# Kernel optimization log

Hardware: AMD Instinct MI355X
Metric: run time of the kernel (lower is better)

The kernel has to match this reference:

```python
import jax, jax.numpy as jnp
import numpy as np

NUM_NODES = 100000
NUM_EDGES = 1600000
NUM_GRAPHS = 64
IN_DIM, HID, NCLS = 64, 128, 10


def setup_inputs() -> dict:
    key = jax.random.key(0)
    ks = jax.random.split(key, 12)
    x = jax.random.normal(ks[0], (NUM_NODES, IN_DIM), dtype=jnp.float32)
    src = jax.random.randint(ks[1], (NUM_EDGES,), 0, NUM_NODES, dtype=jnp.int32)
    dst = jax.random.randint(ks[2], (NUM_EDGES,), 0, NUM_NODES, dtype=jnp.int32)
    batch = jnp.sort(jax.random.randint(ks[3], (NUM_NODES,), 0, NUM_GRAPHS, dtype=jnp.int32))
    def glorot(k, shape):
        lim = (6.0 / (shape[0] + shape[1])) ** 0.5
        return jax.random.uniform(k, shape, jnp.float32, -lim, lim)
    return {
        "x": x, "src": src, "dst": dst, "batch": batch,
        "W1": glorot(ks[4], (IN_DIM, HID)), "b1": jnp.zeros((HID,), jnp.float32),
        "W2": glorot(ks[5], (HID, HID)), "b2": jnp.zeros((HID,), jnp.float32),
        "Wl1": glorot(ks[6], (HID, HID // 2)), "bl1": jnp.zeros((HID // 2,), jnp.float32),
        "Wl2": glorot(ks[7], (HID // 2, NCLS)), "bl2": jnp.zeros((NCLS,), jnp.float32),
    }


def gcn_conv(x, W, b, src, dst):
    # GCNConv: out = D^{-1/2} (A + I) D^{-1/2} (x @ W) + b, deg from A+I
    h = x @ W  # [N, H]
    ones = jnp.ones((src.shape[0],), h.dtype)
    deg = jax.ops.segment_sum(ones, dst, num_segments=NUM_NODES) + 1.0  # +1 self-loop
    dinv = jax.lax.rsqrt(deg)  # [N]
    norm = dinv[src] * dinv[dst]  # [E]
    msg = h[src] * norm[:, None]  # [E, H] gather + scale
    agg = jax.ops.segment_sum(msg, dst, num_segments=NUM_NODES)  # scatter-add
    agg = agg + h * (dinv * dinv)[:, None]  # self-loop message
    return agg + b


def reference(x, src, dst, batch, W1, b1, W2, b2, Wl1, bl1, Wl2, bl2):
    h = jax.nn.relu(gcn_conv(x, W1, b1, src, dst))
    h = jax.nn.relu(gcn_conv(h, W2, b2, src, dst))
    # global mean pool per graph
    sums = jax.ops.segment_sum(h, batch, num_segments=NUM_GRAPHS)  # [G, H]
    cnts = jax.ops.segment_sum(jnp.ones((h.shape[0],), h.dtype), batch, num_segments=NUM_GRAPHS)
    pooled = sums / jnp.maximum(cnts, 1.0)[:, None]
    h = jax.nn.relu(pooled @ Wl1 + bl1)
    return h @ Wl2 + bl2  # [G, num_classes]
```

## Files before the change

### kernel.cpp

```cpp
#include <hip/hip_runtime.h>
#include <hip/hip_bf16.h>

#define NODES_N 100000
#define EDGES_E 1600000
#define GRAPHS_G 64

#define BIN_SHIFT 7
#define BIN_NODES 128
#define NBINS 782
#define NB1 512
#define EPB1 3125

typedef unsigned int uint;
typedef unsigned short ushort;
typedef __attribute__((ext_vector_type(8))) short bf16x8;
typedef __attribute__((ext_vector_type(4))) float f32x4;


__device__ inline uint pack_bf2(float lo, float hi) {
    __hip_bfloat162 h2 = __float22bfloat162_rn(make_float2(lo, hi));
    return *reinterpret_cast<uint*>(&h2);
}

__device__ inline void acc_bf2(uint w, float& a0, float& a1) {
    a0 += __uint_as_float(w << 16);
    a1 += __uint_as_float(w & 0xffff0000u);
}

__device__ inline ushort f2bf(float v) {
    __hip_bfloat16 b = __float2bfloat16(v);
    return *reinterpret_cast<ushort*>(&b);
}


__global__ __launch_bounds__(256) void p1_hist_k(const int* __restrict__ dst,
                                                 int* __restrict__ hist_t) {
    __shared__ int h[NBINS];
    for (int i = threadIdx.x; i < NBINS; i += 256) h[i] = 0;
    __syncthreads();
    int b = blockIdx.x;
    int e0 = b * EPB1, e1 = min(EDGES_E, e0 + EPB1);
    for (int e = e0 + threadIdx.x; e < e1; e += 256)
        atomicAdd(&h[dst[e] >> BIN_SHIFT], 1);
    __syncthreads();
    for (int i = threadIdx.x; i < NBINS; i += 256)
        hist_t[i * NB1 + b] = h[i];
}

__global__ __launch_bounds__(256) void p1_scanbins_k(int* __restrict__ hist_t,
                                                     int* __restrict__ bintot) {
    __shared__ int sd[256];
    __shared__ int carry;
    int bin = blockIdx.x, t = threadIdx.x;
    if (t == 0) carry = 0;
    __syncthreads();
    int* row = hist_t + bin * NB1;
    for (int base = 0; base < NB1; base += 256) {
        int v = row[base + t];
        sd[t] = v; __syncthreads();
        for (int o = 1; o < 256; o <<= 1) {
            int x = (t >= o) ? sd[t - o] : 0;
            __syncthreads();
            sd[t] += x;
            __syncthreads();
        }
        row[base + t] = carry + sd[t] - v;
        __syncthreads();
        if (t == 255) carry += sd[255];
        __syncthreads();
    }
    if (t == 0) bintot[bin] = carry;
}

__global__ __launch_bounds__(1024) void binstart_k(const int* __restrict__ bintot,
                                                   int* __restrict__ binstart,
                                                   int* __restrict__ rowptr) {
    __shared__ int sd[1024];
    int t = threadIdx.x;
    int v = (t < NBINS) ? bintot[t] : 0;
    sd[t] = v; __syncthreads();
    for (int o = 1; o < 1024; o <<= 1) {
        int x = (t >= o) ? sd[t - o] : 0;
        __syncthreads();
        sd[t] += x;
        __syncthreads();
    }
    if (t < NBINS) binstart[t] = sd[t] - v;
    if (t == 0) { binstart[NBINS] = EDGES_E; rowptr[NODES_N] = EDGES_E; }
}

__global__ __launch_bounds__(256) void p1_scatter_k(const int* __restrict__ src,
                                                    const int* __restrict__ dst,
                                                    const int* __restrict__ hist_t,
                                                    const int* __restrict__ binstart,
                                                    uint* __restrict__ pairs) {
    __shared__ int cur[NBINS];
    int b = blockIdx.x;
    for (int i = threadIdx.x; i < NBINS; i += 256)
        cur[i] = binstart[i] + hist_t[i * NB1 + b];
    __syncthreads();
    int e0 = b * EPB1, e1 = min(EDGES_E, e0 + EPB1);
    for (int e = e0 + threadIdx.x; e < e1; e += 256) {
        int d = dst[e];
        int pos = atomicAdd(&cur[d >> BIN_SHIFT], 1);
        pairs[pos] = ((uint)src[e] << BIN_SHIFT) | (uint)(d & (BIN_NODES - 1));
    }
}

__global__ __launch_bounds__(256) void p2_build_k(const uint* __restrict__ pairs,
                                                  const int* __restrict__ binstart,
                                                  int* __restrict__ colidx,
                                                  int* __restrict__ rowptr,
                                                  float* __restrict__ dinv) {
    __shared__ int h[BIN_NODES];
    __shared__ int off[BIN_NODES];
    __shared__ int cur[BIN_NODES];
    int bin = blockIdx.x, t = threadIdx.x;
    int node0 = bin << BIN_SHIFT;
    if (t < BIN_NODES) h[t] = 0;
    __syncthreads();
    int e0 = binstart[bin], e1 = binstart[bin + 1];
    for (int e = e0 + t; e < e1; e += 256)
        atomicAdd(&h[pairs[e] & (BIN_NODES - 1)], 1);
    __syncthreads();
    if (t < BIN_NODES) off[t] = h[t];
    __syncthreads();
    for (int o = 1; o < BIN_NODES; o <<= 1) {
        int x = (t < BIN_NODES && t >= o) ? off[t - o] : 0;
        __syncthreads();
        if (t < BIN_NODES) off[t] += x;
        __syncthreads();
    }
    if (t < BIN_NODES) {
        int excl = off[t] - h[t];
        cur[t] = e0 + excl;
        int node = node0 + t;
        if (node < NODES_N) {
            rowptr[node] = e0 + excl;
            dinv[node] = rsqrtf((float)h[t] + 1.0f);
        }
    }
    __syncthreads();
    for (int e = e0 + t; e < e1; e += 256) {
        uint p = pairs[e];
        int pos = atomicAdd(&cur[p & (BIN_NODES - 1)], 1);
        colidx[pos] = (int)(p >> BIN_SHIFT);
    }
}


__global__ __launch_bounds__(256) void scale_x_k(const float* __restrict__ x,
                                                 const float* __restrict__ dinv,
                                                 uint* __restrict__ xt, int n) {
    int gid = blockIdx.x * blockDim.x + threadIdx.x;
    if (gid >= n * 8) return;
    int row = gid >> 3, l = gid & 7;
    float dv = dinv[row];
    const float* p = &x[(size_t)row * 64 + l * 8];
    float4 a = *(const float4*)p;
    float4 b = *(const float4*)(p + 4);
    uint4 o;
    o.x = pack_bf2(a.x * dv, a.y * dv);
    o.y = pack_bf2(a.z * dv, a.w * dv);
    o.z = pack_bf2(b.x * dv, b.y * dv);
    o.w = pack_bf2(b.z * dv, b.w * dv);
    *(uint4*)&xt[(size_t)row * 32 + l * 4] = o;
}


__global__ __launch_bounds__(256) void gather64_k(const uint* __restrict__ xt,
                                                  const int* __restrict__ rowptr,
                                                  const int* __restrict__ colidx,
                                                  uint* __restrict__ st, int n) {
    int lane = threadIdx.x & 7;
    int local = threadIdx.x >> 3;
    int co = lane * 4;
    for (int node = blockIdx.x * 32 + local; node < n; node += gridDim.x * 32) {
        float a0=0,a1=0,a2=0,a3=0,a4=0,a5=0,a6=0,a7=0;
        uint4 v = *(const uint4*)&xt[(size_t)node * 32 + co];
        acc_bf2(v.x, a0, a1); acc_bf2(v.y, a2, a3);
        acc_bf2(v.z, a4, a5); acc_bf2(v.w, a6, a7);
        int beg = rowptr[node], end = rowptr[node + 1];
        int e = beg;
        for (; e + 3 < end; e += 4) {
            int s0 = colidx[e], s1 = colidx[e+1], s2 = colidx[e+2], s3 = colidx[e+3];
            uint4 v0 = *(const uint4*)&xt[(size_t)s0 * 32 + co];
            uint4 v1 = *(const uint4*)&xt[(size_t)s1 * 32 + co];
            uint4 v2 = *(const uint4*)&xt[(size_t)s2 * 32 + co];
            uint4 v3 = *(const uint4*)&xt[(size_t)s3 * 32 + co];
            acc_bf2(v0.x,a0,a1); acc_bf2(v0.y,a2,a3); acc_bf2(v0.z,a4,a5); acc_bf2(v0.w,a6,a7);
            acc_bf2(v1.x,a0,a1); acc_bf2(v1.y,a2,a3); acc_bf2(v1.z,a4,a5); acc_bf2(v1.w,a6,a7);
            acc_bf2(v2.x,a0,a1); acc_bf2(v2.y,a2,a3); acc_bf2(v2.z,a4,a5); acc_bf2(v2.w,a6,a7);
            acc_bf2(v3.x,a0,a1); acc_bf2(v3.y,a2,a3); acc_bf2(v3.z,a4,a5); acc_bf2(v3.w,a6,a7);
        }
        for (; e < end; e++) {
            uint4 v0 = *(const uint4*)&xt[(size_t)colidx[e] * 32 + co];
            acc_bf2(v0.x,a0,a1); acc_bf2(v0.y,a2,a3); acc_bf2(v0.z,a4,a5); acc_bf2(v0.w,a6,a7);
        }
        uint4 o;
        o.x = pack_bf2(a0, a1);
        o.y = pack_bf2(a2, a3);
        o.z = pack_bf2(a4, a5);
        o.w = pack_bf2(a6, a7);
        *(uint4*)&st[(size_t)node * 32 + co] = o;
    }
}


template <int P>
__global__ __launch_bounds__(256) void gather128_k(const uint* __restrict__ hp,
                                                   const int* __restrict__ rowptr,
                                                   const int* __restrict__ colidx,
                                                   const float* __restrict__ dinv,
                                                   const float* __restrict__ bias,
                                                   uint* __restrict__ h2b, int n) {
    int lane = threadIdx.x & 7;
    int local = threadIdx.x >> 3;
    int co = P * 32 + lane * 4;
    for (int node = blockIdx.x * 32 + local; node < n; node += gridDim.x * 32) {
        float a0=0,a1=0,a2=0,a3=0,a4=0,a5=0,a6=0,a7=0;
        uint4 v = *(const uint4*)&hp[(size_t)node * 64 + co];
        acc_bf2(v.x, a0, a1); acc_bf2(v.y, a2, a3);
        acc_bf2(v.z, a4, a5); acc_bf2(v.w, a6, a7);
        int beg = rowptr[node], end = rowptr[node + 1];
        int e = beg;
        for (; e + 3 < end; e += 4) {
            int s0 = colidx[e], s1 = colidx[e+1], s2 = colidx[e+2], s3 = colidx[e+3];
            uint4 v0 = *(const uint4*)&hp[(size_t)s0 * 64 + co];
            uint4 v1 = *(const uint4*)&hp[(size_t)s1 * 64 + co];
            uint4 v2 = *(const uint4*)&hp[(size_t)s2 * 64 + co];
            uint4 v3 = *(const uint4*)&hp[(size_t)s3 * 64 + co];
            acc_bf2(v0.x,a0,a1); acc_bf2(v0.y,a2,a3); acc_bf2(v0.z,a4,a5); acc_bf2(v0.w,a6,a7);
            acc_bf2(v1.x,a0,a1); acc_bf2(v1.y,a2,a3); acc_bf2(v1.z,a4,a5); acc_bf2(v1.w,a6,a7);
            acc_bf2(v2.x,a0,a1); acc_bf2(v2.y,a2,a3); acc_bf2(v2.z,a4,a5); acc_bf2(v2.w,a6,a7);
            acc_bf2(v3.x,a0,a1); acc_bf2(v3.y,a2,a3); acc_bf2(v3.z,a4,a5); acc_bf2(v3.w,a6,a7);
        }
        for (; e < end; e++) {
            uint4 v0 = *(const uint4*)&hp[(size_t)colidx[e] * 64 + co];
            acc_bf2(v0.x,a0,a1); acc_bf2(v0.y,a2,a3); acc_bf2(v0.z,a4,a5); acc_bf2(v0.w,a6,a7);
        }
        float dv = dinv[node];
        int jb = P * 64 + lane * 8;
        float4 b0 = *(const float4*)&bias[jb];
        float4 b1 = *(const float4*)&bias[jb + 4];
        float o0 = fmaxf(fmaf(dv, a0, b0.x), 0.f);
        float o1 = fmaxf(fmaf(dv, a1, b0.y), 0.f);
        float o2 = fmaxf(fmaf(dv, a2, b0.z), 0.f);
        float o3 = fmaxf(fmaf(dv, a3, b0.w), 0.f);
        float o4 = fmaxf(fmaf(dv, a4, b1.x), 0.f);
        float o5 = fmaxf(fmaf(dv, a5, b1.y), 0.f);
        float o6 = fmaxf(fmaf(dv, a6, b1.z), 0.f);
        float o7 = fmaxf(fmaf(dv, a7, b1.w), 0.f);
        uint4 ov;
        ov.x = pack_bf2(o0, o1);
        ov.y = pack_bf2(o2, o3);
        ov.z = pack_bf2(o4, o5);
        ov.w = pack_bf2(o6, o7);
        *(uint4*)&h2b[(size_t)node * 64 + co] = ov;
    }
}


__device__ inline void pack_w_one(const float* W, ushort* Wf, int gid, int KS) {
    int j = gid & 7, l = (gid >> 3) & 63, f = gid >> 9;
    int nt = f / KS, ks = f - nt * KS;
    int k = ks * 32 + ((l >> 4) & 3) * 8 + j;
    int n = nt * 16 + (l & 15);
    Wf[gid] = f2bf(W[k * 128 + n]);
}

__global__ void pack_w_both_k(const float* __restrict__ W1, ushort* __restrict__ W1f,
                              const float* __restrict__ W2, ushort* __restrict__ W2f) {
    int gid = blockIdx.x * 256 + threadIdx.x;
    if (gid < 8192) pack_w_one(W1, W1f, gid, 2);
    else if (gid < 8192 + 16384) pack_w_one(W2, W2f, gid - 8192, 4);
}


template <int K, int EPI>
__global__ __launch_bounds__(256) void gemm_mfma_k(const ushort* __restrict__ A,
                                                   const ushort* __restrict__ Wf,
                                                   const float* __restrict__ dinv,
                                                   const float* __restrict__ bias,
                                                   ushort* __restrict__ outb, int n) {
    constexpr int KS = K / 32;
    int wave = threadIdx.x >> 6;
    int lane = threadIdx.x & 63;
    int row0 = (blockIdx.x * 4 + wave) * 16;
    if (row0 >= n) return;
    int m = lane & 15, g = lane >> 4;
    int arow = min(row0 + m, n - 1);

    bf16x8 a[KS];
    const ushort* abase = &A[(size_t)arow * K + g * 8];
#pragma unroll
    for (int ks = 0; ks < KS; ks++)
        a[ks] = *reinterpret_cast<const bf16x8*>(abase + ks * 32);

    f32x4 acc[8];
#pragma unroll
    for (int nt = 0; nt < 8; nt++) {
        acc[nt] = (f32x4){0.f, 0.f, 0.f, 0.f};
#pragma unroll
        for (int ks = 0; ks < KS; ks++) {
            bf16x8 b = *reinterpret_cast<const bf16x8*>(&Wf[((size_t)(nt * KS + ks) * 64 + lane) * 8]);
            acc[nt] = __builtin_amdgcn_mfma_f32_16x16x32_bf16(a[ks], b, acc[nt], 0, 0, 0);
        }
    }

    int orow0 = row0 + g * 4;
#pragma unroll
    for (int r = 0; r < 4; r++) {
        int row = orow0 + r;
        if (row < n) {
            float dvr = dinv[row];
#pragma unroll
            for (int nt = 0; nt < 8; nt++) {
                float v = acc[nt][r] * dvr;
                if (EPI == 0) v = fmaxf(v + bias[nt * 16 + m], 0.f);
                outb[(size_t)row * 128 + nt * 16 + m] = f2bf(v);
            }
        }
    }
}


__global__ __launch_bounds__(128) void pool_k(const uint* __restrict__ h2b,
                                              const int* __restrict__ batch, int n,
                                              float* __restrict__ sums, float* __restrict__ cnts) {
    int j = threadIdx.x;
    int wj = j >> 1;
    int hi = j & 1;
    int chunk = (n + gridDim.x - 1) / gridDim.x;
    int i0 = blockIdx.x * chunk;
    int i1 = min(n, i0 + chunk);
    if (i0 >= n) return;
    int cur = batch[i0];
    float acc = 0.f;
    int cnt = 0;
    for (int i = i0; i < i1; i++) {
        int g = batch[i];
        if (g != cur) {
            atomicAdd(&sums[cur * 128 + j], acc);
            if (j == 0) atomicAdd(&cnts[cur], (float)cnt);
            acc = 0.f; cnt = 0; cur = g;
        }
        uint w = h2b[(size_t)i * 64 + wj];
        acc += __uint_as_float(hi ? (w & 0xffff0000u) : (w << 16));
        cnt++;
    }
    atomicAdd(&sums[cur * 128 + j], acc);
    if (j == 0) atomicAdd(&cnts[cur], (float)cnt);
}


__global__ __launch_bounds__(64) void mlp_k(const float* __restrict__ sums, const float* __restrict__ cnts,
                                            const float* __restrict__ Wl1, const float* __restrict__ bl1,
                                            const float* __restrict__ Wl2, const float* __restrict__ bl2,
                                            float* __restrict__ out) {
    __shared__ float pooled[128];
    __shared__ float hidden[64];
    int g = blockIdx.x, t = threadIdx.x;
    float c = fmaxf(cnts[g], 1.0f);
    pooled[t]      = sums[g * 128 + t] / c;
    pooled[t + 64] = sums[g * 128 + 64 + t] / c;
    __syncthreads();
    float a = bl1[t];
#pragma unroll 4
    for (int cc = 0; cc < 128; cc++) a = fmaf(pooled[cc], Wl1[cc * 64 + t], a);
    hidden[t] = fmaxf(a, 0.f);
    __syncthreads();
    if (t < 10) {
        float o = bl2[t];
#pragma unroll 8
        for (int jj = 0; jj < 64; jj++) o = fmaf(hidden[jj], Wl2[jj * 10 + t], o);
        out[g * 10 + t] = o;
    }
}


extern "C" void kernel_launch(void* const* d_in, const int* in_sizes, int n_in,
                              void* d_out, int out_size, void* d_ws, size_t ws_size,
                              hipStream_t stream) {
    const float* x    = (const float*)d_in[0];
    const int*   src  = (const int*)d_in[1];
    const int*   dst  = (const int*)d_in[2];
    const int*   batch= (const int*)d_in[3];
    const float* W1   = (const float*)d_in[4];
    const float* b1   = (const float*)d_in[5];
    const float* W2   = (const float*)d_in[6];
    const float* b2   = (const float*)d_in[7];
    const float* Wl1  = (const float*)d_in[8];
    const float* bl1  = (const float*)d_in[9];
    const float* Wl2  = (const float*)d_in[10];
    const float* bl2  = (const float*)d_in[11];
    float* out = (float*)d_out;

    const int N = NODES_N;

    size_t off = 0;
    auto take = [&](size_t bytes) { size_t o = off; off = (off + bytes + 255) & ~(size_t)255; return o; };
    char* ws = (char*)d_ws;
    ushort* h1b  = (ushort*)(ws + take((size_t)N * 128 * 2));
    uint*   h2p  = (uint*)(ws + take((size_t)N * 128 * 2));
    size_t  shbytes = (size_t)N * 64 * 2;
    char*   shreg = ws + take(shbytes);
    uint*   pairs = (uint*)shreg;
    uint*   stil  = (uint*)shreg;
    uint*   xt   = (uint*)(ws + take((size_t)N * 64 * 2));
    float*  dinv = (float*)(ws + take((size_t)N * 4));
    ushort* W1f  = (ushort*)(ws + take((size_t)64 * 128 * 2));
    ushort* W2f  = (ushort*)(ws + take((size_t)128 * 128 * 2));
    size_t zbytes = ((size_t)GRAPHS_G * 128 + GRAPHS_G) * 4;
    char*  zbase  = ws + take(zbytes);
    float* sums   = (float*)zbase;
    float* cnts   = (float*)(zbase + (size_t)GRAPHS_G * 128 * 4);
    int*   rowptr = (int*)(ws + take((size_t)(N + 1) * 4));
    int*   colidx = (int*)(ws + take((size_t)EDGES_E * 4));
    int*   hist_t = (int*)(ws + take((size_t)NBINS * NB1 * 4));
    int*   bintot = (int*)(ws + take((size_t)NBINS * 4));
    int*   binstart = (int*)(ws + take((size_t)(NBINS + 1) * 4));
    uint*  h2b = (uint*)h1b;
    (void)ws_size; (void)in_sizes; (void)n_in; (void)out_size;

    hipMemsetAsync(zbase, 0, zbytes, stream);

    pack_w_both_k<<<(8192 + 16384 + 255) / 256, 256, 0, stream>>>(W1, W1f, W2, W2f);

    p1_hist_k<<<NB1, 256, 0, stream>>>(dst, hist_t);
    p1_scanbins_k<<<NBINS, 256, 0, stream>>>(hist_t, bintot);
    binstart_k<<<1, 1024, 0, stream>>>(bintot, binstart, rowptr);
    p1_scatter_k<<<NB1, 256, 0, stream>>>(src, dst, hist_t, binstart, pairs);
    p2_build_k<<<NBINS, 256, 0, stream>>>(pairs, binstart, colidx, rowptr, dinv);

    scale_x_k<<<(N * 8 + 255) / 256, 256, 0, stream>>>(x, dinv, xt, N);
    gather64_k<<<2048, 256, 0, stream>>>(xt, rowptr, colidx, stil, N);
    int gblk = (N + 63) / 64;
    gemm_mfma_k<64, 0><<<gblk, 256, 0, stream>>>((const ushort*)stil, W1f, dinv, b1, h1b, N);

    gemm_mfma_k<128, 1><<<gblk, 256, 0, stream>>>(h1b, W2f, dinv, nullptr, (ushort*)h2p, N);
    int g128 = (N + 31) / 32;
    gather128_k<0><<<g128, 256, 0, stream>>>(h2p, rowptr, colidx, dinv, b2, h2b, N);
    gather128_k<1><<<g128, 256, 0, stream>>>(h2p, rowptr, colidx, dinv, b2, h2b, N);

    pool_k<<<1024, 128, 0, stream>>>(h2b, batch, N, sums, cnts);
    mlp_k<<<GRAPHS_G, 64, 0, stream>>>(sums, cnts, Wl1, bl1, Wl2, bl2, out);
}
```

Before: 236.9 us.

## Fuse x scaling into CSR build and gather64 into layer-1 MFMA GEMM

The dinv scaling and bf16 packing of x now happen at the end of p2_build_k, which drops the separate scale_x kernel. The layer-1 neighbor gather is folded into the MFMA GEMM: each lane aggregates the 16 features it feeds into the MFMA A operand, so the intermediate gathered buffer never goes through global memory. The weight packing and the zeroing of the pool accumulators are merged into one kernel that replaces the memset. The cost is that the fused gather assigns one node per 4 lanes with 2×16B loads each, which changes the memory access granularity and occupancy compared with the 8-lanes-per-node gather.

```diff
diff --git a/kernel.cpp b/kernel.cpp
--- a/kernel.cpp
+++ b/kernel.cpp
@@ -30,6 +30,27 @@
 __device__ inline ushort f2bf(float v) {
     __hip_bfloat16 b = __float2bfloat16(v);
     return *reinterpret_cast<ushort*>(&b);
+}
+
+
+__device__ inline void pack_w_one(const float* W, ushort* Wf, int gid, int KS) {
+    int j = gid & 7, l = (gid >> 3) & 63, f = gid >> 9;
+    int nt = f / KS, ks = f - nt * KS;
+    int k = ks * 32 + ((l >> 4) & 3) * 8 + j;
+    int n = nt * 16 + (l & 15);
+    Wf[gid] = f2bf(W[k * 128 + n]);
+}
+
+__global__ void pack_w_zero_k(const float* __restrict__ W1, ushort* __restrict__ W1f,
+                              const float* __restrict__ W2, ushort* __restrict__ W2f,
+                              float* __restrict__ zf) {
+    int gid = blockIdx.x * 256 + threadIdx.x;
+    if (gid < 8192) pack_w_one(W1, W1f, gid, 2);
+    else if (gid < 24576) pack_w_one(W2, W2f, gid - 8192, 4);
+    else {
+        int i = gid - 24576;
+        if (i < GRAPHS_G * 128 + GRAPHS_G) zf[i] = 0.f;
+    }
 }
 
 
@@ -109,12 +130,15 @@
 
 __global__ __launch_bounds__(256) void p2_build_k(const uint* __restrict__ pairs,
                                                   const int* __restrict__ binstart,
+                                                  const float* __restrict__ x,
                                                   int* __restrict__ colidx,
                                                   int* __restrict__ rowptr,
-                                                  float* __restrict__ dinv) {
+                                                  float* __restrict__ dinv,
+                                                  uint* __restrict__ xt) {
     __shared__ int h[BIN_NODES];
     __shared__ int off[BIN_NODES];
     __shared__ int cur[BIN_NODES];
+    __shared__ float ldv[BIN_NODES];
     int bin = blockIdx.x, t = threadIdx.x;
     int node0 = bin << BIN_SHIFT;
     if (t < BIN_NODES) h[t] = 0;
@@ -126,18 +150,20 @@
     if (t < BIN_NODES) off[t] = h[t];
     __syncthreads();
     for (int o = 1; o < BIN_NODES; o <<= 1) {
-        int x = (t < BIN_NODES && t >= o) ? off[t - o] : 0;
-        __syncthreads();
-        if (t < BIN_NODES) off[t] += x;
+        int x2 = (t < BIN_NODES && t >= o) ? off[t - o] : 0;
+        __syncthreads();
+        if (t < BIN_NODES) off[t] += x2;
         __syncthreads();
     }
     if (t < BIN_NODES) {
         int excl = off[t] - h[t];
         cur[t] = e0 + excl;
+        float dv = rsqrtf((float)h[t] + 1.0f);
+        ldv[t] = dv;
         int node = node0 + t;
         if (node < NODES_N) {
             rowptr[node] = e0 + excl;
-            dinv[node] = rsqrtf((float)h[t] + 1.0f);
+            dinv[node] = dv;
         }
     }
     __syncthreads();
@@ -146,63 +172,128 @@
         int pos = atomicAdd(&cur[p & (BIN_NODES - 1)], 1);
         colidx[pos] = (int)(p >> BIN_SHIFT);
     }
-}
-
-
-__global__ __launch_bounds__(256) void scale_x_k(const float* __restrict__ x,
-                                                 const float* __restrict__ dinv,
-                                                 uint* __restrict__ xt, int n) {
-    int gid = blockIdx.x * blockDim.x + threadIdx.x;
-    if (gid >= n * 8) return;
-    int row = gid >> 3, l = gid & 7;
-    float dv = dinv[row];
-    const float* p = &x[(size_t)row * 64 + l * 8];
-    float4 a = *(const float4*)p;
-    float4 b = *(const float4*)(p + 4);
-    uint4 o;
-    o.x = pack_bf2(a.x * dv, a.y * dv);
-    o.y = pack_bf2(a.z * dv, a.w * dv);
-    o.z = pack_bf2(b.x * dv, b.y * dv);
-    o.w = pack_bf2(b.z * dv, b.w * dv);
-    *(uint4*)&xt[(size_t)row * 32 + l * 4] = o;
-}
-
-
-__global__ __launch_bounds__(256) void gather64_k(const uint* __restrict__ xt,
-                                                  const int* __restrict__ rowptr,
-                                                  const int* __restrict__ colidx,
-                                                  uint* __restrict__ st, int n) {
-    int lane = threadIdx.x & 7;
-    int local = threadIdx.x >> 3;
-    int co = lane * 4;
-    for (int node = blockIdx.x * 32 + local; node < n; node += gridDim.x * 32) {
-        float a0=0,a1=0,a2=0,a3=0,a4=0,a5=0,a6=0,a7=0;
-        uint4 v = *(const uint4*)&xt[(size_t)node * 32 + co];
-        acc_bf2(v.x, a0, a1); acc_bf2(v.y, a2, a3);
-        acc_bf2(v.z, a4, a5); acc_bf2(v.w, a6, a7);
-        int beg = rowptr[node], end = rowptr[node + 1];
-        int e = beg;
-        for (; e + 3 < end; e += 4) {
-            int s0 = colidx[e], s1 = colidx[e+1], s2 = colidx[e+2], s3 = colidx[e+3];
-            uint4 v0 = *(const uint4*)&xt[(size_t)s0 * 32 + co];
-            uint4 v1 = *(const uint4*)&xt[(size_t)s1 * 32 + co];
-            uint4 v2 = *(const uint4*)&xt[(size_t)s2 * 32 + co];
-            uint4 v3 = *(const uint4*)&xt[(size_t)s3 * 32 + co];
-            acc_bf2(v0.x,a0,a1); acc_bf2(v0.y,a2,a3); acc_bf2(v0.z,a4,a5); acc_bf2(v0.w,a6,a7);
-            acc_bf2(v1.x,a0,a1); acc_bf2(v1.y,a2,a3); acc_bf2(v1.z,a4,a5); acc_bf2(v1.w,a6,a7);
-            acc_bf2(v2.x,a0,a1); acc_bf2(v2.y,a2,a3); acc_bf2(v2.z,a4,a5); acc_bf2(v2.w,a6,a7);
-            acc_bf2(v3.x,a0,a1); acc_bf2(v3.y,a2,a3); acc_bf2(v3.z,a4,a5); acc_bf2(v3.w,a6,a7);
-        }
-        for (; e < end; e++) {
-            uint4 v0 = *(const uint4*)&xt[(size_t)colidx[e] * 32 + co];
-            acc_bf2(v0.x,a0,a1); acc_bf2(v0.y,a2,a3); acc_bf2(v0.z,a4,a5); acc_bf2(v0.w,a6,a7);
-        }
-        uint4 o;
-        o.x = pack_bf2(a0, a1);
-        o.y = pack_bf2(a2, a3);
-        o.z = pack_bf2(a4, a5);
-        o.w = pack_bf2(a6, a7);
-        *(uint4*)&st[(size_t)node * 32 + co] = o;
+    int nmax = min(NODES_N - node0, BIN_NODES);
+    for (int i = t; i < nmax * 16; i += 256) {
+        int nl = i >> 4, c = i & 15;
+        int node = node0 + nl;
+        float dv = ldv[nl];
+        float4 v = *(const float4*)&x[(size_t)node * 64 + c * 4];
+        uint2 o = make_uint2(pack_bf2(v.x * dv, v.y * dv), pack_bf2(v.z * dv, v.w * dv));
+        *(uint2*)&xt[(size_t)node * 32 + c * 2] = o;
+    }
+}
+
+
+__global__ __launch_bounds__(256) void conv1_fused_k(const uint* __restrict__ xt,
+                                                     const int* __restrict__ rowptr,
+                                                     const int* __restrict__ colidx,
+                                                     const float* __restrict__ dinv,
+                                                     const float* __restrict__ bias,
+                                                     const ushort* __restrict__ Wf,
+                                                     ushort* __restrict__ h1b, int n) {
+    int wave = threadIdx.x >> 6;
+    int lane = threadIdx.x & 63;
+    int row0 = (blockIdx.x * 4 + wave) * 16;
+    if (row0 >= n) return;
+    int m = lane & 15, g = lane >> 4;
+    int node = min(row0 + m, n - 1);
+    int g4 = g * 4;
+
+    float s[16];
+#pragma unroll
+    for (int i = 0; i < 16; i++) s[i] = 0.f;
+
+    auto accrow = [&](int r) {
+        uint4 vA = *(const uint4*)&xt[(size_t)r * 32 + g4];
+        uint4 vB = *(const uint4*)&xt[(size_t)r * 32 + 16 + g4];
+        acc_bf2(vA.x, s[0], s[1]);  acc_bf2(vA.y, s[2], s[3]);
+        acc_bf2(vA.z, s[4], s[5]);  acc_bf2(vA.w, s[6], s[7]);
+        acc_bf2(vB.x, s[8], s[9]);  acc_bf2(vB.y, s[10], s[11]);
+        acc_bf2(vB.z, s[12], s[13]); acc_bf2(vB.w, s[14], s[15]);
+    };
+
+    accrow(node);
+    int beg = rowptr[node], end = rowptr[node + 1];
+    int e = beg;
+    for (; e + 3 < end; e += 4) {
+        int s0 = colidx[e], s1 = colidx[e + 1], s2 = colidx[e + 2], s3 = colidx[e + 3];
+        accrow(s0); accrow(s1); accrow(s2); accrow(s3);
+    }
+    for (; e < end; e++) accrow(colidx[e]);
+
+    uint4 u0 = make_uint4(pack_bf2(s[0], s[1]), pack_bf2(s[2], s[3]),
+                          pack_bf2(s[4], s[5]), pack_bf2(s[6], s[7]));
+    uint4 u1 = make_uint4(pack_bf2(s[8], s[9]), pack_bf2(s[10], s[11]),
+                          pack_bf2(s[12], s[13]), pack_bf2(s[14], s[15]));
+    bf16x8 a0 = *reinterpret_cast<bf16x8*>(&u0);
+    bf16x8 a1 = *reinterpret_cast<bf16x8*>(&u1);
+
+    f32x4 acc[8];
+#pragma unroll
+    for (int nt = 0; nt < 8; nt++) {
+        acc[nt] = (f32x4){0.f, 0.f, 0.f, 0.f};
+        bf16x8 b0 = *reinterpret_cast<const bf16x8*>(&Wf[((size_t)(nt * 2 + 0) * 64 + lane) * 8]);
+        bf16x8 b1 = *reinterpret_cast<const bf16x8*>(&Wf[((size_t)(nt * 2 + 1) * 64 + lane) * 8]);
+        acc[nt] = __builtin_amdgcn_mfma_f32_16x16x32_bf16(a0, b0, acc[nt], 0, 0, 0);
+        acc[nt] = __builtin_amdgcn_mfma_f32_16x16x32_bf16(a1, b1, acc[nt], 0, 0, 0);
+    }
+
+    int orow0 = row0 + g * 4;
+#pragma unroll
+    for (int r = 0; r < 4; r++) {
+        int row = orow0 + r;
+        if (row < n) {
+            float dvr = dinv[row];
+#pragma unroll
+            for (int nt = 0; nt < 8; nt++) {
+                float v = fmaxf(fmaf(dvr, acc[nt][r], bias[nt * 16 + m]), 0.f);
+                h1b[(size_t)row * 128 + nt * 16 + m] = f2bf(v);
+            }
+        }
+    }
+}
+
+
+template <int K>
+__global__ __launch_bounds__(256) void gemm_mfma_k(const ushort* __restrict__ A,
+                                                   const ushort* __restrict__ Wf,
+                                                   const float* __restrict__ dinv,
+                                                   ushort* __restrict__ outb, int n) {
+    constexpr int KS = K / 32;
+    int wave = threadIdx.x >> 6;
+    int lane = threadIdx.x & 63;
+    int row0 = (blockIdx.x * 4 + wave) * 16;
+    if (row0 >= n) return;
+    int m = lane & 15, g = lane >> 4;
+    int arow = min(row0 + m, n - 1);
+
+    bf16x8 a[KS];
+    const ushort* abase = &A[(size_t)arow * K + g * 8];
+#pragma unroll
+    for (int ks = 0; ks < KS; ks++)
+        a[ks] = *reinterpret_cast<const bf16x8*>(abase + ks * 32);
+
+    f32x4 acc[8];
+#pragma unroll
+    for (int nt = 0; nt < 8; nt++) {
+        acc[nt] = (f32x4){0.f, 0.f, 0.f, 0.f};
+#pragma unroll
+        for (int ks = 0; ks < KS; ks++) {
+            bf16x8 b = *reinterpret_cast<const bf16x8*>(&Wf[((size_t)(nt * KS + ks) * 64 + lane) * 8]);
+            acc[nt] = __builtin_amdgcn_mfma_f32_16x16x32_bf16(a[ks], b, acc[nt], 0, 0, 0);
+        }
+    }
+
+    int orow0 = row0 + g * 4;
+#pragma unroll
+    for (int r = 0; r < 4; r++) {
+        int row = orow0 + r;
+        if (row < n) {
+            float dvr = dinv[row];
+#pragma unroll
+            for (int nt = 0; nt < 8; nt++)
+                outb[(size_t)row * 128 + nt * 16 + m] = f2bf(acc[nt][r] * dvr);
+        }
     }
 }
 
@@ -261,70 +352,6 @@
 }
 
 
-__device__ inline void pack_w_one(const float* W, ushort* Wf, int gid, int KS) {
-    int j = gid & 7, l = (gid >> 3) & 63, f = gid >> 9;
-    int nt = f / KS, ks = f - nt * KS;
-    int k = ks * 32 + ((l >> 4) & 3) * 8 + j;
-    int n = nt * 16 + (l & 15);
-    Wf[gid] = f2bf(W[k * 128 + n]);
-}
-
-__global__ void pack_w_both_k(const float* __restrict__ W1, ushort* __restrict__ W1f,
-                              const float* __restrict__ W2, ushort* __restrict__ W2f) {
-    int gid = blockIdx.x * 256 + threadIdx.x;
-    if (gid < 8192) pack_w_one(W1, W1f, gid, 2);
-    else if (gid < 8192 + 16384) pack_w_one(W2, W2f, gid - 8192, 4);
-}
-
-
-template <int K, int EPI>
-__global__ __launch_bounds__(256) void gemm_mfma_k(const ushort* __restrict__ A,
-                                                   const ushort* __restrict__ Wf,
-                                                   const float* __restrict__ dinv,
-                                                   const float* __restrict__ bias,
-                                                   ushort* __restrict__ outb, int n) {
-    constexpr int KS = K / 32;
-    int wave = threadIdx.x >> 6;
-    int lane = threadIdx.x & 63;
-    int row0 = (blockIdx.x * 4 + wave) * 16;
-    if (row0 >= n) return;
-    int m = lane & 15, g = lane >> 4;
-    int arow = min(row0 + m, n - 1);
-
-    bf16x8 a[KS];
-    const ushort* abase = &A[(size_t)arow * K + g * 8];
-#pragma unroll
-    for (int ks = 0; ks < KS; ks++)
-        a[ks] = *reinterpret_cast<const bf16x8*>(abase + ks * 32);
-
-    f32x4 acc[8];
-#pragma unroll
-    for (int nt = 0; nt < 8; nt++) {
-        acc[nt] = (f32x4){0.f, 0.f, 0.f, 0.f};
-#pragma unroll
-        for (int ks = 0; ks < KS; ks++) {
-            bf16x8 b = *reinterpret_cast<const bf16x8*>(&Wf[((size_t)(nt * KS + ks) * 64 + lane) * 8]);
-            acc[nt] = __builtin_amdgcn_mfma_f32_16x16x32_bf16(a[ks], b, acc[nt], 0, 0, 0);
-        }
-    }
-
-    int orow0 = row0 + g * 4;
-#pragma unroll
-    for (int r = 0; r < 4; r++) {
-        int row = orow0 + r;
-        if (row < n) {
-            float dvr = dinv[row];
-#pragma unroll
-            for (int nt = 0; nt < 8; nt++) {
-                float v = acc[nt][r] * dvr;
-                if (EPI == 0) v = fmaxf(v + bias[nt * 16 + m], 0.f);
-                outb[(size_t)row * 128 + nt * 16 + m] = f2bf(v);
-            }
-        }
-    }
-}
-
-
 __global__ __launch_bounds__(128) void pool_k(const uint* __restrict__ h2b,
                                               const int* __restrict__ batch, int n,
                                               float* __restrict__ sums, float* __restrict__ cnts) {
@@ -403,10 +430,7 @@
     char* ws = (char*)d_ws;
     ushort* h1b  = (ushort*)(ws + take((size_t)N * 128 * 2));
     uint*   h2p  = (uint*)(ws + take((size_t)N * 128 * 2));
-    size_t  shbytes = (size_t)N * 64 * 2;
-    char*   shreg = ws + take(shbytes);
-    uint*   pairs = (uint*)shreg;
-    uint*   stil  = (uint*)shreg;
+    uint*   pairs = (uint*)(ws + take((size_t)EDGES_E * 4));
     uint*   xt   = (uint*)(ws + take((size_t)N * 64 * 2));
     float*  dinv = (float*)(ws + take((size_t)N * 4));
     ushort* W1f  = (ushort*)(ws + take((size_t)64 * 128 * 2));
@@ -423,22 +447,19 @@
     uint*  h2b = (uint*)h1b;
     (void)ws_size; (void)in_sizes; (void)n_in; (void)out_size;
 
-    hipMemsetAsync(zbase, 0, zbytes, stream);
-
-    pack_w_both_k<<<(8192 + 16384 + 255) / 256, 256, 0, stream>>>(W1, W1f, W2, W2f);
+    pack_w_zero_k<<<(24576 + GRAPHS_G * 128 + GRAPHS_G + 255) / 256, 256, 0, stream>>>(
+        W1, W1f, W2, W2f, sums);
 
     p1_hist_k<<<NB1, 256, 0, stream>>>(dst, hist_t);
     p1_scanbins_k<<<NBINS, 256, 0, stream>>>(hist_t, bintot);
     binstart_k<<<1, 1024, 0, stream>>>(bintot, binstart, rowptr);
     p1_scatter_k<<<NB1, 256, 0, stream>>>(src, dst, hist_t, binstart, pairs);
-    p2_build_k<<<NBINS, 256, 0, stream>>>(pairs, binstart, colidx, rowptr, dinv);
-
-    scale_x_k<<<(N * 8 + 255) / 256, 256, 0, stream>>>(x, dinv, xt, N);
-    gather64_k<<<2048, 256, 0, stream>>>(xt, rowptr, colidx, stil, N);
+    p2_build_k<<<NBINS, 256, 0, stream>>>(pairs, binstart, x, colidx, rowptr, dinv, xt);
+
     int gblk = (N + 63) / 64;
-    gemm_mfma_k<64, 0><<<gblk, 256, 0, stream>>>((const ushort*)stil, W1f, dinv, b1, h1b, N);
-
-    gemm_mfma_k<128, 1><<<gblk, 256, 0, stream>>>(h1b, W2f, dinv, nullptr, (ushort*)h2p, N);
+    conv1_fused_k<<<gblk, 256, 0, stream>>>(xt, rowptr, colidx, dinv, b1, W1f, h1b, N);
+
+    gemm_mfma_k<128><<<gblk, 256, 0, stream>>>(h1b, W2f, dinv, (ushort*)h2p, N);
     int g128 = (N + 31) / 32;
     gather128_k<0><<<g128, 256, 0, stream>>>(h2p, rowptr, colidx, dinv, b2, h2b, N);
     gather128_k<1><<<g128, 256, 0, stream>>>(h2p, rowptr, colidx, dinv, b2, h2b, N);
```

Result: no change. 235.7 us (-0.5%).

## Fuse layer GEMMs, fold x scaling into CSR build, merge launches

Applied to the files above, without the earlier changes.

The two MFMA GEMMs become one kernel that keeps the layer-1 output in LDS and feeds it straight into the layer-2 GEMM, so the h1 round trip through global memory goes away. The dinv scaling and bf16 packing of x now happen inside p2_build_k, and the memset is folded into the weight-packing kernel. The two gather128 launches become a single 2D grid, and the gather kernels move from grid-stride loops to one node per thread group. Together these cut kernel launches and intermediate traffic, at the cost of more registers and LDS in the fused GEMM.

```diff
diff --git a/kernel.cpp b/kernel.cpp
--- a/kernel.cpp
+++ b/kernel.cpp
@@ -30,6 +30,29 @@
 __device__ inline ushort f2bf(float v) {
     __hip_bfloat16 b = __float2bfloat16(v);
     return *reinterpret_cast<ushort*>(&b);
+}
+
+
+__device__ inline void pack_w_one(const float* W, ushort* Wf, int gid, int KS) {
+    int j = gid & 7, l = (gid >> 3) & 63, f = gid >> 9;
+    int nt = f / KS, ks = f - nt * KS;
+    int k = ks * 32 + ((l >> 4) & 3) * 8 + j;
+    int n = nt * 16 + (l & 15);
+    Wf[gid] = f2bf(W[k * 128 + n]);
+}
+
+#define NZERO (GRAPHS_G * 128 + GRAPHS_G)
+
+__global__ void pack_w_zero_k(const float* __restrict__ W1, ushort* __restrict__ W1f,
+                              const float* __restrict__ W2, ushort* __restrict__ W2f,
+                              float* __restrict__ zf) {
+    int gid = blockIdx.x * 256 + threadIdx.x;
+    if (gid < 8192) pack_w_one(W1, W1f, gid, 2);
+    else if (gid < 24576) pack_w_one(W2, W2f, gid - 8192, 4);
+    else {
+        int i = gid - 24576;
+        if (i < NZERO) zf[i] = 0.f;
+    }
 }
 
 
@@ -109,12 +132,15 @@
 
 __global__ __launch_bounds__(256) void p2_build_k(const uint* __restrict__ pairs,
                                                   const int* __restrict__ binstart,
+                                                  const float* __restrict__ x,
                                                   int* __restrict__ colidx,
                                                   int* __restrict__ rowptr,
-                                                  float* __restrict__ dinv) {
+                                                  float* __restrict__ dinv,
+                                                  uint* __restrict__ xt) {
     __shared__ int h[BIN_NODES];
     __shared__ int off[BIN_NODES];
     __shared__ int cur[BIN_NODES];
+    __shared__ float ldv[BIN_NODES];
     int bin = blockIdx.x, t = threadIdx.x;
     int node0 = bin << BIN_SHIFT;
     if (t < BIN_NODES) h[t] = 0;
@@ -126,18 +152,20 @@
     if (t < BIN_NODES) off[t] = h[t];
     __syncthreads();
     for (int o = 1; o < BIN_NODES; o <<= 1) {
-        int x = (t < BIN_NODES && t >= o) ? off[t - o] : 0;
-        __syncthreads();
-        if (t < BIN_NODES) off[t] += x;
+        int x2 = (t < BIN_NODES && t >= o) ? off[t - o] : 0;
+        __syncthreads();
+        if (t < BIN_NODES) off[t] += x2;
         __syncthreads();
     }
     if (t < BIN_NODES) {
         int excl = off[t] - h[t];
         cur[t] = e0 + excl;
+        float dv = rsqrtf((float)h[t] + 1.0f);
+        ldv[t] = dv;
         int node = node0 + t;
         if (node < NODES_N) {
             rowptr[node] = e0 + excl;
-            dinv[node] = rsqrtf((float)h[t] + 1.0f);
+            dinv[node] = dv;
         }
     }
     __syncthreads();
@@ -146,25 +174,15 @@
         int pos = atomicAdd(&cur[p & (BIN_NODES - 1)], 1);
         colidx[pos] = (int)(p >> BIN_SHIFT);
     }
-}
-
-
-__global__ __launch_bounds__(256) void scale_x_k(const float* __restrict__ x,
-                                                 const float* __restrict__ dinv,
-                                                 uint* __restrict__ xt, int n) {
-    int gid = blockIdx.x * blockDim.x + threadIdx.x;
-    if (gid >= n * 8) return;
-    int row = gid >> 3, l = gid & 7;
-    float dv = dinv[row];
-    const float* p = &x[(size_t)row * 64 + l * 8];
-    float4 a = *(const float4*)p;
-    float4 b = *(const float4*)(p + 4);
-    uint4 o;
-    o.x = pack_bf2(a.x * dv, a.y * dv);
-    o.y = pack_bf2(a.z * dv, a.w * dv);
-    o.z = pack_bf2(b.x * dv, b.y * dv);
-    o.w = pack_bf2(b.z * dv, b.w * dv);
-    *(uint4*)&xt[(size_t)row * 32 + l * 4] = o;
+    int nmax = min(NODES_N - node0, BIN_NODES);
+    for (int i = t; i < nmax * 16; i += 256) {
+        int nl = i >> 4, c = i & 15;
+        int node = node0 + nl;
+        float dv = ldv[nl];
+        float4 v = *(const float4*)&x[(size_t)node * 64 + c * 4];
+        uint2 o = make_uint2(pack_bf2(v.x * dv, v.y * dv), pack_bf2(v.z * dv, v.w * dv));
+        *(uint2*)&xt[(size_t)node * 32 + c * 2] = o;
+    }
 }
 
 
@@ -175,7 +193,9 @@
     int lane = threadIdx.x & 7;
     int local = threadIdx.x >> 3;
     int co = lane * 4;
-    for (int node = blockIdx.x * 32 + local; node < n; node += gridDim.x * 32) {
+    int node = blockIdx.x * 32 + local;
+    if (node >= n) return;
+    {
         float a0=0,a1=0,a2=0,a3=0,a4=0,a5=0,a6=0,a7=0;
         uint4 v = *(const uint4*)&xt[(size_t)node * 32 + co];
         acc_bf2(v.x, a0, a1); acc_bf2(v.y, a2, a3);
@@ -207,17 +227,90 @@
 }
 
 
-template <int P>
+__global__ __launch_bounds__(256) void gemm_dual_k(const ushort* __restrict__ A,
+                                                   const ushort* __restrict__ W1f,
+                                                   const ushort* __restrict__ W2f,
+                                                   const float* __restrict__ dinv,
+                                                   const float* __restrict__ b1,
+                                                   ushort* __restrict__ h2p, int n) {
+    __shared__ ushort hl[4][16][132];
+    int wave = threadIdx.x >> 6;
+    int lane = threadIdx.x & 63;
+    int row0 = (blockIdx.x * 4 + wave) * 16;
+    if (row0 >= n) return;
+    int m = lane & 15, g = lane >> 4;
+    int arow = min(row0 + m, n - 1);
+
+    const ushort* ab = &A[(size_t)arow * 64 + g * 8];
+    bf16x8 a0 = *reinterpret_cast<const bf16x8*>(ab);
+    bf16x8 a1 = *reinterpret_cast<const bf16x8*>(ab + 32);
+    f32x4 acc[8];
+#pragma unroll
+    for (int nt = 0; nt < 8; nt++) {
+        acc[nt] = (f32x4){0.f, 0.f, 0.f, 0.f};
+        bf16x8 w0 = *reinterpret_cast<const bf16x8*>(&W1f[((size_t)(nt * 2 + 0) * 64 + lane) * 8]);
+        bf16x8 w1 = *reinterpret_cast<const bf16x8*>(&W1f[((size_t)(nt * 2 + 1) * 64 + lane) * 8]);
+        acc[nt] = __builtin_amdgcn_mfma_f32_16x16x32_bf16(a0, w0, acc[nt], 0, 0, 0);
+        acc[nt] = __builtin_amdgcn_mfma_f32_16x16x32_bf16(a1, w1, acc[nt], 0, 0, 0);
+    }
+
+    int orow0 = row0 + g * 4;
+#pragma unroll
+    for (int r = 0; r < 4; r++) {
+        float dvr = dinv[min(orow0 + r, n - 1)];
+#pragma unroll
+        for (int nt = 0; nt < 8; nt++) {
+            float v = fmaxf(fmaf(dvr, acc[nt][r], b1[nt * 16 + m]), 0.f);
+            hl[wave][g * 4 + r][nt * 16 + m] = f2bf(v);
+        }
+    }
+
+    bf16x8 hfrag[4];
+#pragma unroll
+    for (int ks = 0; ks < 4; ks++) {
+        uint2 lo = *(const uint2*)&hl[wave][m][g * 8 + ks * 32];
+        uint2 hi = *(const uint2*)&hl[wave][m][g * 8 + ks * 32 + 4];
+        uint4 u = make_uint4(lo.x, lo.y, hi.x, hi.y);
+        hfrag[ks] = *reinterpret_cast<bf16x8*>(&u);
+    }
+
+    f32x4 acc2[8];
+#pragma unroll
+    for (int nt = 0; nt < 8; nt++) {
+        acc2[nt] = (f32x4){0.f, 0.f, 0.f, 0.f};
+#pragma unroll
+        for (int ks = 0; ks < 4; ks++) {
+            bf16x8 w = *reinterpret_cast<const bf16x8*>(&W2f[((size_t)(nt * 4 + ks) * 64 + lane) * 8]);
+            acc2[nt] = __builtin_amdgcn_mfma_f32_16x16x32_bf16(hfrag[ks], w, acc2[nt], 0, 0, 0);
+        }
+    }
+
+#pragma unroll
+    for (int r = 0; r < 4; r++) {
+        int row = orow0 + r;
+        if (row < n) {
+            float dvr = dinv[row];
+#pragma unroll
+            for (int nt = 0; nt < 8; nt++)
+                h2p[(size_t)row * 128 + nt * 16 + m] = f2bf(acc2[nt][r] * dvr);
+        }
+    }
+}
+
+
 __global__ __launch_bounds__(256) void gather128_k(const uint* __restrict__ hp,
                                                    const int* __restrict__ rowptr,
                                                    const int* __restrict__ colidx,
                                                    const float* __restrict__ dinv,
                                                    const float* __restrict__ bias,
                                                    uint* __restrict__ h2b, int n) {
+    int P = blockIdx.y;
     int lane = threadIdx.x & 7;
     int local = threadIdx.x >> 3;
     int co = P * 32 + lane * 4;
-    for (int node = blockIdx.x * 32 + local; node < n; node += gridDim.x * 32) {
+    int node = blockIdx.x * 32 + local;
+    if (node >= n) return;
+    {
         float a0=0,a1=0,a2=0,a3=0,a4=0,a5=0,a6=0,a7=0;
         uint4 v = *(const uint4*)&hp[(size_t)node * 64 + co];
         acc_bf2(v.x, a0, a1); acc_bf2(v.y, a2, a3);
@@ -257,70 +350,6 @@
         ov.z = pack_bf2(o4, o5);
         ov.w = pack_bf2(o6, o7);
         *(uint4*)&h2b[(size_t)node * 64 + co] = ov;
-    }
-}
-
-
-__device__ inline void pack_w_one(const float* W, ushort* Wf, int gid, int KS) {
-    int j = gid & 7, l = (gid >> 3) & 63, f = gid >> 9;
-    int nt = f / KS, ks = f - nt * KS;
-    int k = ks * 32 + ((l >> 4) & 3) * 8 + j;
-    int n = nt * 16 + (l & 15);
-    Wf[gid] = f2bf(W[k * 128 + n]);
-}
-
-__global__ void pack_w_both_k(const float* __restrict__ W1, ushort* __restrict__ W1f,
-                              const float* __restrict__ W2, ushort* __restrict__ W2f) {
-    int gid = blockIdx.x * 256 + threadIdx.x;
-    if (gid < 8192) pack_w_one(W1, W1f, gid, 2);
-    else if (gid < 8192 + 16384) pack_w_one(W2, W2f, gid - 8192, 4);
-}
-
-
-template <int K, int EPI>
-__global__ __launch_bounds__(256) void gemm_mfma_k(const ushort* __restrict__ A,
-                                                   const ushort* __restrict__ Wf,
-                                                   const float* __restrict__ dinv,
-                                                   const float* __restrict__ bias,
-                                                   ushort* __restrict__ outb, int n) {
-    constexpr int KS = K / 32;
-    int wave = threadIdx.x >> 6;
-    int lane = threadIdx.x & 63;
-    int row0 = (blockIdx.x * 4 + wave) * 16;
-    if (row0 >= n) return;
-    int m = lane & 15, g = lane >> 4;
-    int arow = min(row0 + m, n - 1);
-
-    bf16x8 a[KS];
-    const ushort* abase = &A[(size_t)arow * K + g * 8];
-#pragma unroll
-    for (int ks = 0; ks < KS; ks++)
-        a[ks] = *reinterpret_cast<const bf16x8*>(abase + ks * 32);
-
-    f32x4 acc[8];
-#pragma unroll
-    for (int nt = 0; nt < 8; nt++) {
-        acc[nt] = (f32x4){0.f, 0.f, 0.f, 0.f};
-#pragma unroll
-        for (int ks = 0; ks < KS; ks++) {
-            bf16x8 b = *reinterpret_cast<const bf16x8*>(&Wf[((size_t)(nt * KS + ks) * 64 + lane) * 8]);
-            acc[nt] = __builtin_amdgcn_mfma_f32_16x16x32_bf16(a[ks], b, acc[nt], 0, 0, 0);
-        }
-    }
-
-    int orow0 = row0 + g * 4;
-#pragma unroll
-    for (int r = 0; r < 4; r++) {
-        int row = orow0 + r;
-        if (row < n) {
-            float dvr = dinv[row];
-#pragma unroll
-            for (int nt = 0; nt < 8; nt++) {
-                float v = acc[nt][r] * dvr;
-                if (EPI == 0) v = fmaxf(v + bias[nt * 16 + m], 0.f);
-                outb[(size_t)row * 128 + nt * 16 + m] = f2bf(v);
-            }
-        }
     }
 }
 
@@ -401,8 +430,8 @@
     size_t off = 0;
     auto take = [&](size_t bytes) { size_t o = off; off = (off + bytes + 255) & ~(size_t)255; return o; };
     char* ws = (char*)d_ws;
-    ushort* h1b  = (ushort*)(ws + take((size_t)N * 128 * 2));
     uint*   h2p  = (uint*)(ws + take((size_t)N * 128 * 2));
+    uint*   h2b  = (uint*)(ws + take((size_t)N * 128 * 2));
     size_t  shbytes = (size_t)N * 64 * 2;
     char*   shreg = ws + take(shbytes);
     uint*   pairs = (uint*)shreg;
@@ -411,7 +440,7 @@
     float*  dinv = (float*)(ws + take((size_t)N * 4));
     ushort* W1f  = (ushort*)(ws + take((size_t)64 * 128 * 2));
     ushort* W2f  = (ushort*)(ws + take((size_t)128 * 128 * 2));
-    size_t zbytes = ((size_t)GRAPHS_G * 128 + GRAPHS_G) * 4;
+    size_t zbytes = (size_t)NZERO * 4;
     char*  zbase  = ws + take(zbytes);
     float* sums   = (float*)zbase;
     float* cnts   = (float*)(zbase + (size_t)GRAPHS_G * 128 * 4);
@@ -420,28 +449,23 @@
     int*   hist_t = (int*)(ws + take((size_t)NBINS * NB1 * 4));
     int*   bintot = (int*)(ws + take((size_t)NBINS * 4));
     int*   binstart = (int*)(ws + take((size_t)(NBINS + 1) * 4));
-    uint*  h2b = (uint*)h1b;
     (void)ws_size; (void)in_sizes; (void)n_in; (void)out_size;
 
-    hipMemsetAsync(zbase, 0, zbytes, stream);
-
-    pack_w_both_k<<<(8192 + 16384 + 255) / 256, 256, 0, stream>>>(W1, W1f, W2, W2f);
+    pack_w_zero_k<<<(24576 + NZERO + 255) / 256, 256, 0, stream>>>(W1, W1f, W2, W2f, sums);
 
     p1_hist_k<<<NB1, 256, 0, stream>>>(dst, hist_t);
     p1_scanbins_k<<<NBINS, 256, 0, stream>>>(hist_t, bintot);
     binstart_k<<<1, 1024, 0, stream>>>(bintot, binstart, rowptr);
     p1_scatter_k<<<NB1, 256, 0, stream>>>(src, dst, hist_t, binstart, pairs);
-    p2_build_k<<<NBINS, 256, 0, stream>>>(pairs, binstart, colidx, rowptr, dinv);
-
-    scale_x_k<<<(N * 8 + 255) / 256, 256, 0, stream>>>(x, dinv, xt, N);
-    gather64_k<<<2048, 256, 0, stream>>>(xt, rowptr, colidx, stil, N);
+    p2_build_k<<<NBINS, 256, 0, stream>>>(pairs, binstart, x, colidx, rowptr, dinv, xt);
+
+    int g32 = (N + 31) / 32;
+    gather64_k<<<g32, 256, 0, stream>>>(xt, rowptr, colidx, stil, N);
+
     int gblk = (N + 63) / 64;
-    gemm_mfma_k<64, 0><<<gblk, 256, 0, stream>>>((const ushort*)stil, W1f, dinv, b1, h1b, N);
-
-    gemm_mfma_k<128, 1><<<gblk, 256, 0, stream>>>(h1b, W2f, dinv, nullptr, (ushort*)h2p, N);
-    int g128 = (N + 31) / 32;
-    gather128_k<0><<<g128, 256, 0, stream>>>(h2p, rowptr, colidx, dinv, b2, h2b, N);
-    gather128_k<1><<<g128, 256, 0, stream>>>(h2p, rowptr, colidx, dinv, b2, h2b, N);
+    gemm_dual_k<<<gblk, 256, 0, stream>>>((const ushort*)stil, W1f, W2f, dinv, b1, (ushort*)h2p, N);
+
+    gather128_k<<<dim3(g32, 2), 256, 0, stream>>>(h2p, rowptr, colidx, dinv, b2, h2b, N);
 
     pool_k<<<1024, 128, 0, stream>>>(h2b, batch, N, sums, cnts);
     mlp_k<<<GRAPHS_G, 64, 0, stream>>>(sums, cnts, Wl1, bl1, Wl2, bl2, out);
```

Measured after the change: 217.5 us. -8.2%, faster.
